# Kernel tuning notes

Measured on AMD Instinct MI355X. Metric: run time of the kernel, lower is better.

Reference implementation:

```python
import jax, jax.numpy as jnp
import numpy as np

N = 2048          # batch*trg_len (B=4, T=512)
B, T = 4, 512
D = 512           # model_dim
V = 32000         # vocab_size
K = 16            # top_k


def setup_inputs() -> dict:
    key = jax.random.key(0)
    ks = jax.random.split(key, 12)
    hidden = jax.random.normal(ks[0], (N, D), dtype=jnp.float32)
    logits = jax.random.normal(ks[1], (N, V), dtype=jnp.float32)
    distances = jax.random.uniform(ks[2], (N, K), dtype=jnp.float32)  # L2 distances >= 0
    searched_hidden = jax.random.normal(ks[3], (N, K, D), dtype=jnp.float32)
    token_indices = jax.random.randint(ks[4], (N, K), 0, V, dtype=jnp.int64)
    s = 1.0 / np.sqrt(2 * D)
    # bandwidth estimator: Linear(2D -> 1), bias init 20 for GaussianKernel
    bw_W = jax.random.uniform(ks[5], (2 * D, 1), minval=-s, maxval=s, dtype=jnp.float32)
    bw_b = jnp.array([20.0], dtype=jnp.float32)
    # mixing weight estimator: Linear(2D->D), ReLU, Linear(D->1)
    mw_W1 = jax.random.uniform(ks[6], (2 * D, D), minval=-s, maxval=s, dtype=jnp.float32)
    mw_b1 = jax.random.uniform(ks[7], (D,), minval=-s, maxval=s, dtype=jnp.float32)
    s2 = 1.0 / np.sqrt(D)
    mw_W2 = jax.random.uniform(ks[8], (D, 1), minval=-s2, maxval=s2, dtype=jnp.float32)
    mw_b2 = jax.random.uniform(ks[9], (1,), minval=-s2, maxval=s2, dtype=jnp.float32)
    return {
        "hidden": hidden, "logits": logits, "distances": distances,
        "searched_hidden": searched_hidden, "token_indices": token_indices,
        "bw_W": bw_W, "bw_b": bw_b,
        "mw_W1": mw_W1, "mw_b1": mw_b1, "mw_W2": mw_W2, "mw_b2": mw_b2,
    }


def reference(hidden, logits, distances, searched_hidden, token_indices,
              bw_W, bw_b, mw_W1, mw_b1, mw_W2, mw_b2):
    # --- bandwidth: sigmoid(Linear([hidden, mean_k searched_hidden])) -> [N, 1]
    mean_hidden = searched_hidden.mean(axis=1)                       # [N, D]
    bw_in = jnp.concatenate([hidden, mean_hidden], axis=-1)          # [N, 2D]
    bandwidth = jax.nn.sigmoid(bw_in @ bw_W + bw_b)                  # [N, 1]

    # --- model distribution over vocab
    model_dist = jax.nn.softmax(logits, axis=-1)                     # [N, V]

    # --- Gaussian kernel, index_type 'L2': scores = -distances / bandwidth
    scores = -distances / bandwidth                                  # [N, K]
    sparse_dist = jax.nn.softmax(scores, axis=-1)                    # [N, K]
    # scatter-add sparse probs into vocab-sized distribution
    rows = jnp.arange(N)[:, None]                                    # [N, 1]
    example_dist = jnp.zeros((N, V), dtype=sparse_dist.dtype).at[rows, token_indices].add(sparse_dist)

    # --- mixing weight MLP on [hidden, prob-weighted searched hidden]
    merged = jnp.einsum('nkd,nk->nd', searched_hidden, sparse_dist)  # [N, D]
    mw_in = jnp.concatenate([hidden, merged], axis=-1)               # [N, 2D]
    h1 = jax.nn.relu(mw_in @ mw_W1 + mw_b1)                          # [N, D]
    mixing = jax.nn.sigmoid(h1 @ mw_W2 + mw_b2)                      # [N, 1]

    mixed = (1.0 - mixing) * model_dist + mixing * example_dist      # [N, V]
    log_probs = jnp.log(mixed).reshape(B, T, V)
    return log_probs
```

## Files before the change

### kernel.cpp

```cpp
#include <hip/hip_runtime.h>
#include <math.h>

#define N_ROWS 2048
#define D_DIM  512
#define V_DIM  32000
#define K_TOP  16

typedef float f32x4 __attribute__((ext_vector_type(4)));

__global__ __launch_bounds__(512, 2) void k_mlp(
    const float* __restrict__ hidden,
    const float* __restrict__ sh,
    const float* __restrict__ dist,
    const float* __restrict__ bwW,
    const float* __restrict__ bwb,
    const float* __restrict__ W1,
    const float* __restrict__ b1,
    const float* __restrict__ W2,
    const float* __restrict__ b2,
    float* __restrict__ sd_out,
    float* __restrict__ mix_out,
    float* __restrict__ l1m_out)
{
  __shared__ float smem[8192];
  const int tid = threadIdx.x;
  const int tx  = tid & 63;
  const int tz  = tid >> 6;
  const int r0  = blockIdx.x * 8;

  {
    const int lane = tx;
    const int row  = r0 + tz;
    const float4* sh4  = (const float4*)(sh + (size_t)row * (K_TOP * D_DIM));
    const float4* hid4 = (const float4*)(hidden + (size_t)row * D_DIM);
    const float4* bwW4 = (const float4*)bwW;

    float4 shvA[K_TOP], shvB[K_TOP];
#pragma unroll
    for (int k = 0; k < K_TOP; ++k) {
      shvA[k] = sh4[k * 128 + lane];
      shvB[k] = sh4[k * 128 + 64 + lane];
    }
    float dv[K_TOP];
#pragma unroll
    for (int k = 0; k < K_TOP; ++k) dv[k] = dist[row * K_TOP + k];

    float4 msA = make_float4(0.f,0.f,0.f,0.f), msB = make_float4(0.f,0.f,0.f,0.f);
#pragma unroll
    for (int k = 0; k < K_TOP; ++k) {
      msA.x += shvA[k].x; msA.y += shvA[k].y; msA.z += shvA[k].z; msA.w += shvA[k].w;
      msB.x += shvB[k].x; msB.y += shvB[k].y; msB.z += shvB[k].z; msB.w += shvB[k].w;
    }
    const float4 h4a = hid4[lane], h4b = hid4[64 + lane];
    float4* A4w = (float4*)smem;
    A4w[tz * 256 + lane]      = h4a;
    A4w[tz * 256 + 64 + lane] = h4b;
    const float4 wa = bwW4[lane],       wb = bwW4[64 + lane];
    const float4 wc = bwW4[128 + lane], wd = bwW4[192 + lane];
    float bp = h4a.x*wa.x + h4a.y*wa.y + h4a.z*wa.z + h4a.w*wa.w
             + h4b.x*wb.x + h4b.y*wb.y + h4b.z*wb.z + h4b.w*wb.w
             + 0.0625f * (msA.x*wc.x + msA.y*wc.y + msA.z*wc.z + msA.w*wc.w
                        + msB.x*wd.x + msB.y*wd.y + msB.z*wd.z + msB.w*wd.w);
#pragma unroll
    for (int off = 32; off > 0; off >>= 1) bp += __shfl_down(bp, off);
    bp = __shfl(bp, 0);
    const float bw = 1.0f / (1.0f + __expf(-(bp + bwb[0])));

    float sc[K_TOP];
    float mx = -1e30f;
#pragma unroll
    for (int k = 0; k < K_TOP; ++k) {
      sc[k] = -dv[k] / bw;
      mx = fmaxf(mx, sc[k]);
    }
    float ssum = 0.0f;
#pragma unroll
    for (int k = 0; k < K_TOP; ++k) { sc[k] = __expf(sc[k] - mx); ssum += sc[k]; }
    const float inv = 1.0f / ssum;
#pragma unroll
    for (int k = 0; k < K_TOP; ++k) sc[k] *= inv;
    if (lane == 0) {
#pragma unroll
      for (int k = 0; k < K_TOP; ++k) sd_out[row * K_TOP + k] = sc[k];
    }

    float4 mgA = make_float4(0.f,0.f,0.f,0.f), mgB = make_float4(0.f,0.f,0.f,0.f);
#pragma unroll
    for (int k = 0; k < K_TOP; ++k) {
      mgA.x = fmaf(sc[k], shvA[k].x, mgA.x); mgA.y = fmaf(sc[k], shvA[k].y, mgA.y);
      mgA.z = fmaf(sc[k], shvA[k].z, mgA.z); mgA.w = fmaf(sc[k], shvA[k].w, mgA.w);
      mgB.x = fmaf(sc[k], shvB[k].x, mgB.x); mgB.y = fmaf(sc[k], shvB[k].y, mgB.y);
      mgB.z = fmaf(sc[k], shvB[k].z, mgB.z); mgB.w = fmaf(sc[k], shvB[k].w, mgB.w);
    }
    A4w[tz * 256 + 128 + lane] = mgA;
    A4w[tz * 256 + 192 + lane] = mgB;
  }
  __syncthreads();

  float acc[8][8];
#pragma unroll
  for (int r = 0; r < 8; ++r)
#pragma unroll
    for (int j = 0; j < 8; ++j) acc[r][j] = 0.0f;

  const float4* A4 = (const float4*)smem;
  const float4* W4 = (const float4*)W1;
  const int kbase = tz * 128;
  for (int kk = 0; kk < 128; kk += 4) {
    const int k0 = kbase + kk;
    float4 a[8];
#pragma unroll
    for (int r = 0; r < 8; ++r) a[r] = A4[r * 256 + (k0 >> 2)];
#pragma unroll
    for (int dk = 0; dk < 4; ++dk) {
      const int k = k0 + dk;
      const float4 wlo = W4[k * 128 + tx * 2];
      const float4 whi = W4[k * 128 + tx * 2 + 1];
#pragma unroll
      for (int r = 0; r < 8; ++r) {
        const float av = (dk == 0) ? a[r].x : (dk == 1) ? a[r].y
                       : (dk == 2) ? a[r].z : a[r].w;
        acc[r][0] = fmaf(av, wlo.x, acc[r][0]);
        acc[r][1] = fmaf(av, wlo.y, acc[r][1]);
        acc[r][2] = fmaf(av, wlo.z, acc[r][2]);
        acc[r][3] = fmaf(av, wlo.w, acc[r][3]);
        acc[r][4] = fmaf(av, whi.x, acc[r][4]);
        acc[r][5] = fmaf(av, whi.y, acc[r][5]);
        acc[r][6] = fmaf(av, whi.z, acc[r][6]);
        acc[r][7] = fmaf(av, whi.w, acc[r][7]);
      }
    }
  }
  __syncthreads();

#define RED_WRITE(set) {                                                     \
  _Pragma("unroll") for (int r = 0; r < 8; ++r) {                            \
    _Pragma("unroll") for (int j = 0; j < 8; ++j) {                          \
      smem[(set) * 4096 + r * 512 + tx + (j << 6)] = acc[r][j]; } } }
#define RED_ADD(set) {                                                       \
  _Pragma("unroll") for (int r = 0; r < 8; ++r) {                            \
    _Pragma("unroll") for (int j = 0; j < 8; ++j) {                          \
      acc[r][j] += smem[(set) * 4096 + r * 512 + tx + (j << 6)]; } } }

  if (tz == 4) { RED_WRITE(0) } else if (tz == 5) { RED_WRITE(1) }
  __syncthreads();
  if (tz == 0) { RED_ADD(0) } else if (tz == 1) { RED_ADD(1) }
  __syncthreads();
  if (tz == 6) { RED_WRITE(0) } else if (tz == 7) { RED_WRITE(1) }
  __syncthreads();
  if (tz == 2) { RED_ADD(0) } else if (tz == 3) { RED_ADD(1) }
  __syncthreads();
  if (tz == 2) { RED_WRITE(0) } else if (tz == 3) { RED_WRITE(1) }
  __syncthreads();
  if (tz == 0) { RED_ADD(0) } else if (tz == 1) { RED_ADD(1) }
  __syncthreads();
  if (tz == 1) { RED_WRITE(0) }
  __syncthreads();

  if (tz == 0) {
    RED_ADD(0)
    const float4* b1v = (const float4*)b1;
    const float4* w2v = (const float4*)W2;
    const float4 blo = b1v[tx * 2], bhi = b1v[tx * 2 + 1];
    const float4 wlo = w2v[tx * 2], whi = w2v[tx * 2 + 1];
#pragma unroll
    for (int r = 0; r < 8; ++r) {
      float s = fmaxf(acc[r][0] + blo.x, 0.f) * wlo.x
              + fmaxf(acc[r][1] + blo.y, 0.f) * wlo.y
              + fmaxf(acc[r][2] + blo.z, 0.f) * wlo.z
              + fmaxf(acc[r][3] + blo.w, 0.f) * wlo.w
              + fmaxf(acc[r][4] + bhi.x, 0.f) * whi.x
              + fmaxf(acc[r][5] + bhi.y, 0.f) * whi.y
              + fmaxf(acc[r][6] + bhi.z, 0.f) * whi.z
              + fmaxf(acc[r][7] + bhi.w, 0.f) * whi.w;
#pragma unroll
      for (int off = 32; off > 0; off >>= 1) s += __shfl_down(s, off);
      if (tx == 0) {
        const float x  = s + b2[0];
        const float mg = 1.0f / (1.0f + __expf(-x));
        mix_out[r0 + r] = mg;
        l1m_out[r0 + r] = logf(1.0f - mg);
      }
    }
  }
#undef RED_WRITE
#undef RED_ADD
}

__global__ __launch_bounds__(1024) void k_out(
    const float* __restrict__ logits,
    const float* __restrict__ sd,
    const float* __restrict__ mix,
    const float* __restrict__ l1m,
    const int* __restrict__ tok,
    float* __restrict__ out)
{
  const int n   = blockIdx.x;
  const int tid = threadIdx.x;
  __shared__ float Ms[16], Ss[16];
  __shared__ float cSh, LSh;

  float fx_x = 0.f, fx_e = 0.f, fx_m = 0.f, l1m_n = 0.f;
  int fx_my = 0; bool fx_first = false;
  if (tid < K_TOP) {
    fx_my = tok[n * K_TOP + tid];
    fx_first = true;
#pragma unroll
    for (int k2 = 0; k2 < K_TOP; ++k2) {
      const int i2 = tok[n * K_TOP + k2];
      if (i2 == fx_my) { fx_e += sd[n * K_TOP + k2]; if (k2 < tid) fx_first = false; }
    }
    fx_x = logits[(size_t)n * V_DIM + fx_my];
    fx_m = mix[n];
    if (tid == 0) l1m_n = l1m[n];
  }

  const f32x4* in4 = (const f32x4*)(logits + (size_t)n * V_DIM);
  f32x4*      out4 = (f32x4*)(out + (size_t)n * V_DIM);

  f32x4 v[8];
  float tmax = -1e30f;
#pragma unroll
  for (int i = 0; i < 8; ++i) {
    const int idx = tid + (i << 10);
    if (idx < 8000) v[i] = __builtin_nontemporal_load(in4 + idx);
    else { v[i].x = -1e30f; v[i].y = -1e30f; v[i].z = -1e30f; v[i].w = -1e30f; }
    tmax = fmaxf(tmax, fmaxf(fmaxf(v[i].x, v[i].y), fmaxf(v[i].z, v[i].w)));
  }
  float tsum = 0.0f;
#pragma unroll
  for (int i = 0; i < 8; ++i) {
    tsum += __expf(v[i].x - tmax) + __expf(v[i].y - tmax)
          + __expf(v[i].z - tmax) + __expf(v[i].w - tmax);
  }
#pragma unroll
  for (int off = 32; off > 0; off >>= 1) {
    const float M2 = __shfl_xor(tmax, off);
    const float S2 = __shfl_xor(tsum, off);
    const float Mn = fmaxf(tmax, M2);
    tsum = tsum * __expf(tmax - Mn) + S2 * __expf(M2 - Mn);
    tmax = Mn;
  }
  if ((tid & 63) == 0) { Ms[tid >> 6] = tmax; Ss[tid >> 6] = tsum; }
  __syncthreads();
  if (tid == 0) {
    float M = Ms[0], S = Ss[0];
#pragma unroll
    for (int w = 1; w < 16; ++w) {
      const float Mn = fmaxf(M, Ms[w]);
      S = S * __expf(M - Mn) + Ss[w] * __expf(Ms[w] - Mn);
      M = Mn;
    }
    const float L = M + logf(S);
    LSh = L;
    cSh = l1m_n - L;
  }
  __syncthreads();
  const float c = cSh;
#pragma unroll
  for (int i = 0; i < 8; ++i) {
    const int idx = tid + (i << 10);
    if (idx < 8000) {
      f32x4 o;
      o.x = v[i].x + c; o.y = v[i].y + c; o.z = v[i].z + c; o.w = v[i].w + c;
      __builtin_nontemporal_store(o, out4 + idx);
    }
  }
  __syncthreads();
  if (tid < K_TOP && fx_first) {
    const float p = __expf(fx_x - LSh);
    const float r = logf((1.0f - fx_m) * p + fx_m * fx_e);
    __builtin_nontemporal_store(r, out + (size_t)n * V_DIM + fx_my);
  }
}

extern "C" void kernel_launch(void* const* d_in, const int* in_sizes, int n_in,
                              void* d_out, int out_size, void* d_ws, size_t ws_size,
                              hipStream_t stream)
{
  const float* hidden = (const float*)d_in[0];
  const float* logits = (const float*)d_in[1];
  const float* dist   = (const float*)d_in[2];
  const float* sh     = (const float*)d_in[3];
  const int*   tok    = (const int*)d_in[4];
  const float* bwW    = (const float*)d_in[5];
  const float* bwb    = (const float*)d_in[6];
  const float* W1     = (const float*)d_in[7];
  const float* b1     = (const float*)d_in[8];
  const float* W2     = (const float*)d_in[9];
  const float* b2     = (const float*)d_in[10];
  float* out = (float*)d_out;
  float* ws  = (float*)d_ws;

  float* sdp = ws;
  float* mxp = ws + N_ROWS * K_TOP;
  float* l1p = mxp + N_ROWS;

  k_mlp<<<N_ROWS / 8, 512, 0, stream>>>(hidden, sh, dist, bwW, bwb,
                                        W1, b1, W2, b2, sdp, mxp, l1p);
  k_out<<<N_ROWS, 1024, 0, stream>>>(logits, sdp, mxp, l1p, tok, out);
}
```

Before: 140.7 us.

## Process eight rows per block with double-buffered register prefetch of next row

The output kernel now handles eight rows per 1024-thread block instead of one. It uses two register buffers so the next row's logits load is issued while the current row's softmax reduction finishes and its output is stored. Sparse-token fixups are collected in shared memory and written at the end, after all dense stores. This cuts the grid to 256 blocks and doubles per-thread register use, so occupancy and parallelism are lower in exchange for overlapping loads with compute.

Result: slower. 150.5 us (+6.9%).

```diff
diff --git a/kernel.cpp b/kernel.cpp
--- a/kernel.cpp
+++ b/kernel.cpp
@@ -187,6 +187,93 @@
 #undef RED_ADD
 }
 
+
+__device__ __forceinline__ void row_step(
+    int g, int r0, int tid,
+    const float* __restrict__ logits, const float* __restrict__ sd,
+    const float* __restrict__ mix, const float* __restrict__ l1m,
+    const int* __restrict__ tok, float* __restrict__ out,
+    f32x4 (&vC)[8], f32x4 (&vN)[8],
+    float& fxxC, float& fxeC, float& fxmC, int& fxyC, bool& fxfC,
+    float& fxxN, float& fxeN, float& fxmN, int& fxyN, bool& fxfN,
+    float l1C, float& l1N,
+    float (&Ms)[2][16], float (&Ss)[2][16],
+    int (&fxP)[8][16], float (&fxV)[8][16])
+{
+  const int r = r0 + g;
+
+  float tmax = -1e30f;
+#pragma unroll
+  for (int i = 0; i < 8; ++i)
+    tmax = fmaxf(tmax, fmaxf(fmaxf(vC[i].x, vC[i].y), fmaxf(vC[i].z, vC[i].w)));
+  float tsum = 0.f;
+#pragma unroll
+  for (int i = 0; i < 8; ++i)
+    tsum += __expf(vC[i].x - tmax) + __expf(vC[i].y - tmax)
+          + __expf(vC[i].z - tmax) + __expf(vC[i].w - tmax);
+
+#pragma unroll
+  for (int off = 32; off > 0; off >>= 1) {
+    const float M2 = __shfl_xor(tmax, off);
+    const float S2 = __shfl_xor(tsum, off);
+    const float Mn = fmaxf(tmax, M2);
+    tsum = tsum * __expf(tmax - Mn) + S2 * __expf(M2 - Mn);
+    tmax = Mn;
+  }
+  if ((tid & 63) == 0) { Ms[g & 1][tid >> 6] = tmax; Ss[g & 1][tid >> 6] = tsum; }
+  __syncthreads();
+
+  if (g < 7) {
+    const int pr = r + 1;
+    const f32x4* inN = (const f32x4*)(logits + (size_t)pr * V_DIM);
+#pragma unroll
+    for (int i = 0; i < 8; ++i) {
+      if (i < 7 || tid < 832) vN[i] = __builtin_nontemporal_load(inN + tid + (i << 10));
+      else { vN[i].x = -1e30f; vN[i].y = -1e30f; vN[i].z = -1e30f; vN[i].w = -1e30f; }
+    }
+    l1N = l1m[pr];
+    if (tid < K_TOP) {
+      fxyN = tok[pr * K_TOP + tid];
+      fxfN = true; fxeN = 0.f;
+#pragma unroll
+      for (int k2 = 0; k2 < K_TOP; ++k2) {
+        const int i2 = tok[pr * K_TOP + k2];
+        if (i2 == fxyN) { fxeN += sd[pr * K_TOP + k2]; if (k2 < tid) fxfN = false; }
+      }
+      fxxN = logits[(size_t)pr * V_DIM + fxyN];
+      fxmN = mix[pr];
+    }
+  }
+
+  float M = Ms[g & 1][0], S = Ss[g & 1][0];
+#pragma unroll
+  for (int w = 1; w < 16; ++w) {
+    const float M2 = Ms[g & 1][w], S2 = Ss[g & 1][w];
+    const float Mn = fmaxf(M, M2);
+    S = S * __expf(M - Mn) + S2 * __expf(M2 - Mn);
+    M = Mn;
+  }
+  const float L = M + logf(S);
+  const float c = l1C - L;
+
+  if (tid < K_TOP) {
+    fxP[g][tid] = fxfC ? fxyC : -1;
+    float rv = 0.f;
+    if (fxfC) rv = logf((1.0f - fxmC) * __expf(fxxC - L) + fxmC * fxeC);
+    fxV[g][tid] = rv;
+  }
+
+  f32x4* out4 = (f32x4*)(out + (size_t)r * V_DIM);
+#pragma unroll
+  for (int i = 0; i < 8; ++i) {
+    if (i < 7 || tid < 832) {
+      f32x4 o;
+      o.x = vC[i].x + c; o.y = vC[i].y + c; o.z = vC[i].z + c; o.w = vC[i].w + c;
+      __builtin_nontemporal_store(o, out4 + tid + (i << 10));
+    }
+  }
+}
+
 __global__ __launch_bounds__(1024) void k_out(
     const float* __restrict__ logits,
     const float* __restrict__ sd,
@@ -195,82 +282,52 @@
     const int* __restrict__ tok,
     float* __restrict__ out)
 {
-  const int n   = blockIdx.x;
   const int tid = threadIdx.x;
-  __shared__ float Ms[16], Ss[16];
-  __shared__ float cSh, LSh;
-
-  float fx_x = 0.f, fx_e = 0.f, fx_m = 0.f, l1m_n = 0.f;
-  int fx_my = 0; bool fx_first = false;
-  if (tid < K_TOP) {
-    fx_my = tok[n * K_TOP + tid];
-    fx_first = true;
-#pragma unroll
-    for (int k2 = 0; k2 < K_TOP; ++k2) {
-      const int i2 = tok[n * K_TOP + k2];
-      if (i2 == fx_my) { fx_e += sd[n * K_TOP + k2]; if (k2 < tid) fx_first = false; }
-    }
-    fx_x = logits[(size_t)n * V_DIM + fx_my];
-    fx_m = mix[n];
-    if (tid == 0) l1m_n = l1m[n];
-  }
-
-  const f32x4* in4 = (const f32x4*)(logits + (size_t)n * V_DIM);
-  f32x4*      out4 = (f32x4*)(out + (size_t)n * V_DIM);
-
-  f32x4 v[8];
-  float tmax = -1e30f;
-#pragma unroll
-  for (int i = 0; i < 8; ++i) {
-    const int idx = tid + (i << 10);
-    if (idx < 8000) v[i] = __builtin_nontemporal_load(in4 + idx);
-    else { v[i].x = -1e30f; v[i].y = -1e30f; v[i].z = -1e30f; v[i].w = -1e30f; }
-    tmax = fmaxf(tmax, fmaxf(fmaxf(v[i].x, v[i].y), fmaxf(v[i].z, v[i].w)));
-  }
-  float tsum = 0.0f;
-#pragma unroll
-  for (int i = 0; i < 8; ++i) {
-    tsum += __expf(v[i].x - tmax) + __expf(v[i].y - tmax)
-          + __expf(v[i].z - tmax) + __expf(v[i].w - tmax);
-  }
-#pragma unroll
-  for (int off = 32; off > 0; off >>= 1) {
-    const float M2 = __shfl_xor(tmax, off);
-    const float S2 = __shfl_xor(tsum, off);
-    const float Mn = fmaxf(tmax, M2);
-    tsum = tsum * __expf(tmax - Mn) + S2 * __expf(M2 - Mn);
-    tmax = Mn;
-  }
-  if ((tid & 63) == 0) { Ms[tid >> 6] = tmax; Ss[tid >> 6] = tsum; }
-  __syncthreads();
-  if (tid == 0) {
-    float M = Ms[0], S = Ss[0];
-#pragma unroll
-    for (int w = 1; w < 16; ++w) {
-      const float Mn = fmaxf(M, Ms[w]);
-      S = S * __expf(M - Mn) + Ss[w] * __expf(Ms[w] - Mn);
-      M = Mn;
-    }
-    const float L = M + logf(S);
-    LSh = L;
-    cSh = l1m_n - L;
-  }
-  __syncthreads();
-  const float c = cSh;
-#pragma unroll
-  for (int i = 0; i < 8; ++i) {
-    const int idx = tid + (i << 10);
-    if (idx < 8000) {
-      f32x4 o;
-      o.x = v[i].x + c; o.y = v[i].y + c; o.z = v[i].z + c; o.w = v[i].w + c;
-      __builtin_nontemporal_store(o, out4 + idx);
-    }
-  }
-  __syncthreads();
-  if (tid < K_TOP && fx_first) {
-    const float p = __expf(fx_x - LSh);
-    const float r = logf((1.0f - fx_m) * p + fx_m * fx_e);
-    __builtin_nontemporal_store(r, out + (size_t)n * V_DIM + fx_my);
+  const int r0  = blockIdx.x * 8;
+  __shared__ float Ms[2][16], Ss[2][16];
+  __shared__ int   fxP[8][16];
+  __shared__ float fxV[8][16];
+
+  f32x4 vA[8], vB[8];
+  float fxxA = 0.f, fxeA = 0.f, fxmA = 0.f; int fxyA = 0; bool fxfA = false;
+  float fxxB = 0.f, fxeB = 0.f, fxmB = 0.f; int fxyB = 0; bool fxfB = false;
+  float l1A = 0.f, l1B = 0.f;
+
+  {
+    const f32x4* in0 = (const f32x4*)(logits + (size_t)r0 * V_DIM);
+#pragma unroll
+    for (int i = 0; i < 8; ++i) {
+      if (i < 7 || tid < 832) vA[i] = __builtin_nontemporal_load(in0 + tid + (i << 10));
+      else { vA[i].x = -1e30f; vA[i].y = -1e30f; vA[i].z = -1e30f; vA[i].w = -1e30f; }
+    }
+    l1A = l1m[r0];
+    if (tid < K_TOP) {
+      fxyA = tok[r0 * K_TOP + tid];
+      fxfA = true;
+#pragma unroll
+      for (int k2 = 0; k2 < K_TOP; ++k2) {
+        const int i2 = tok[r0 * K_TOP + k2];
+        if (i2 == fxyA) { fxeA += sd[r0 * K_TOP + k2]; if (k2 < tid) fxfA = false; }
+      }
+      fxxA = logits[(size_t)r0 * V_DIM + fxyA];
+      fxmA = mix[r0];
+    }
+  }
+
+  for (int gg = 0; gg < 4; ++gg) {
+    row_step(2 * gg,     r0, tid, logits, sd, mix, l1m, tok, out,
+             vA, vB, fxxA, fxeA, fxmA, fxyA, fxfA,
+             fxxB, fxeB, fxmB, fxyB, fxfB, l1A, l1B, Ms, Ss, fxP, fxV);
+    row_step(2 * gg + 1, r0, tid, logits, sd, mix, l1m, tok, out,
+             vB, vA, fxxB, fxeB, fxmB, fxyB, fxfB,
+             fxxA, fxeA, fxmA, fxyA, fxfA, l1B, l1A, Ms, Ss, fxP, fxV);
+  }
+
+  __syncthreads();
+  if (tid < 128) {
+    const int g = tid >> 4, k = tid & 15;
+    const int p = fxP[g][k];
+    if (p >= 0) out[(size_t)(r0 + g) * V_DIM + p] = fxV[g][k];
   }
 }
 
@@ -298,5 +355,5 @@
 
   k_mlp<<<N_ROWS / 8, 512, 0, stream>>>(hidden, sh, dist, bwW, bwb,
                                         W1, b1, W2, b2, sdp, mxp, l1p);
-  k_out<<<N_ROWS, 1024, 0, stream>>>(logits, sdp, mxp, l1p, tok, out);
+  k_out<<<N_ROWS / 8, 1024, 0, stream>>>(logits, sdp, mxp, l1p, tok, out);
 }
```
